# Optimization experiments

Hardware: AMD Instinct MI355X
Metric: run time of the kernel (lower is better)

The kernel has to match this reference:

```python
import jax, jax.numpy as jnp
import numpy as np

N = 100000   # nodes
E = 1000000  # edges
DIN = 128    # atom_in_features
DE = 16      # edge_attr_dim
H = 128      # hidden width (preprocess/cheb/postprocess)
K = 3        # Chebyshev order
EPS = 1e-5


def setup_inputs() -> dict:
    key = jax.random.key(0)
    ks = jax.random.split(key, 16)
    s = 0.02
    return {
        "x": jax.random.normal(ks[0], (N, DIN), jnp.float32),
        "edge_index": jax.random.randint(ks[1], (2, E), 0, N),
        "edge_attr": jax.random.normal(ks[2], (E, DE), jnp.float32),
        # AtomEdgeInteraction linear: (DIN+DE) -> H
        "w_int": jax.random.normal(ks[3], (DIN + DE, H), jnp.float32) * s,
        "b_int": jnp.zeros((H,), jnp.float32),
        # preprocess layer 1: Linear + BatchNorm + ReLU
        "w_pre": jax.random.normal(ks[4], (H, H), jnp.float32) * s,
        "b_pre": jnp.zeros((H,), jnp.float32),
        "g_pre": jnp.ones((H,), jnp.float32),
        "be_pre": jnp.zeros((H,), jnp.float32),
        # ChebConv layers: weight [K, in, out] + bias
        "cheb1_w": jax.random.normal(ks[5], (K, H, H), jnp.float32) * s,
        "cheb1_b": jnp.zeros((H,), jnp.float32),
        "cheb2_w": jax.random.normal(ks[6], (K, H, H), jnp.float32) * s,
        "cheb2_b": jnp.zeros((H,), jnp.float32),
        # postprocess: Linear + BatchNorm + ReLU
        "w_post": jax.random.normal(ks[7], (H, H), jnp.float32) * s,
        "b_post": jnp.zeros((H,), jnp.float32),
        "g_post": jnp.ones((H,), jnp.float32),
        "be_post": jnp.zeros((H,), jnp.float32),
        # output layer H -> 1
        "w_out": jax.random.normal(ks[8], (H, 1), jnp.float32) * s,
        "b_out": jnp.zeros((1,), jnp.float32),
    }


def _bn(z, g, b):
    # BatchNorm1d, training-mode batch statistics (biased variance, like torch)
    m = z.mean(0)
    v = ((z - m) ** 2).mean(0)
    return g * (z - m) * jax.lax.rsqrt(v + EPS) + b


def _cheb(h, W, b, row, col, norm):
    # ChebConv with sym normalization, lambda_max=2 => L_hat = -D^{-1/2} A D^{-1/2}
    def lhat(z):
        return jax.ops.segment_sum(norm[:, None] * z[row], col, num_segments=N)

    Tx0 = h
    out = Tx0 @ W[0]
    Tx1 = lhat(Tx0)
    out = out + Tx1 @ W[1]
    for k in range(2, W.shape[0]):
        Tx2 = 2.0 * lhat(Tx1) - Tx0
        out = out + Tx2 @ W[k]
        Tx0, Tx1 = Tx1, Tx2
    return out + b


def reference(x, edge_index, edge_attr,
              w_int, b_int,
              w_pre, b_pre, g_pre, be_pre,
              cheb1_w, cheb1_b, cheb2_w, cheb2_b,
              w_post, b_post, g_post, be_post,
              w_out, b_out):
    row, col = edge_index[0], edge_index[1]
    ones_e = jnp.ones((E,), x.dtype)

    # AtomEdgeInteraction: gather -> concat -> linear -> scatter_mean over col
    comb = jnp.concatenate([x[row], edge_attr], axis=-1)  # [E, DIN+DE]
    upd = comb @ w_int + b_int                             # [E, H]
    cnt = jax.ops.segment_sum(ones_e, col, num_segments=N)
    h = jax.ops.segment_sum(upd, col, num_segments=N) / jnp.clip(cnt, 1.0)[:, None]

    # preprocess layer 1 (Linear + BN + ReLU; dropout rate 0)
    h = jax.nn.relu(_bn(h @ w_pre + b_pre, g_pre, be_pre))

    # sym-normalized edge coefficients for scaled Laplacian
    deg = jax.ops.segment_sum(ones_e, row, num_segments=N)
    dis = jnp.where(deg > 0, jax.lax.rsqrt(jnp.maximum(deg, 1.0)), 0.0)
    norm = -dis[row] * dis[col]  # [E]

    h = jax.nn.relu(_cheb(h, cheb1_w, cheb1_b, row, col, norm))
    h = jax.nn.relu(_cheb(h, cheb2_w, cheb2_b, row, col, norm))

    # postprocess (Linear + BN + ReLU)
    h = jax.nn.relu(_bn(h @ w_post + b_post, g_post, be_post))

    # output layer, squeeze(-1) -> [N]
    return (h @ w_out + b_out).squeeze(-1)
```

## Files before the change

### kernel.cpp

```cpp
#include <hip/hip_runtime.h>
#include <hip/hip_bf16.h>

using u16 = unsigned short;
using u32 = unsigned int;

#define NN 100000
#define NE 1000000

typedef __attribute__((ext_vector_type(8))) short bfrag;
typedef __attribute__((ext_vector_type(4))) float ffrag;

#define BF16ONE2 0x3F803F80u

__device__ __forceinline__ float bf2f(u16 u) { return __uint_as_float(((u32)u) << 16); }
__device__ __forceinline__ u16 f2bf(float f) {
  u32 x = __float_as_uint(f);
  return (u16)((x + 0x7fffu + ((x >> 16) & 1u)) >> 16);
}
__device__ __forceinline__ float rdv(const void* p, long i, int f) {
  return f ? bf2f(((const u16*)p)[i]) : ((const float*)p)[i];
}
__device__ __forceinline__ void acc8(float* a, uint4 v, float w) {
  a[0] = fmaf(w, __uint_as_float(v.x << 16), a[0]);
  a[1] = fmaf(w, __uint_as_float(v.x & 0xffff0000u), a[1]);
  a[2] = fmaf(w, __uint_as_float(v.y << 16), a[2]);
  a[3] = fmaf(w, __uint_as_float(v.y & 0xffff0000u), a[3]);
  a[4] = fmaf(w, __uint_as_float(v.z << 16), a[4]);
  a[5] = fmaf(w, __uint_as_float(v.z & 0xffff0000u), a[5]);
  a[6] = fmaf(w, __uint_as_float(v.w << 16), a[6]);
  a[7] = fmaf(w, __uint_as_float(v.w & 0xffff0000u), a[7]);
}
__device__ __forceinline__ void acc8bn(float* a, uint4 v, float w, const float* A,
                                       const float* Bb) {
  float x;
  x = __uint_as_float(v.x << 16);
  a[0] = fmaf(w, fmaxf(fmaf(A[0], x, Bb[0]), 0.f), a[0]);
  x = __uint_as_float(v.x & 0xffff0000u);
  a[1] = fmaf(w, fmaxf(fmaf(A[1], x, Bb[1]), 0.f), a[1]);
  x = __uint_as_float(v.y << 16);
  a[2] = fmaf(w, fmaxf(fmaf(A[2], x, Bb[2]), 0.f), a[2]);
  x = __uint_as_float(v.y & 0xffff0000u);
  a[3] = fmaf(w, fmaxf(fmaf(A[3], x, Bb[3]), 0.f), a[3]);
  x = __uint_as_float(v.z << 16);
  a[4] = fmaf(w, fmaxf(fmaf(A[4], x, Bb[4]), 0.f), a[4]);
  x = __uint_as_float(v.z & 0xffff0000u);
  a[5] = fmaf(w, fmaxf(fmaf(A[5], x, Bb[5]), 0.f), a[5]);
  x = __uint_as_float(v.w << 16);
  a[6] = fmaf(w, fmaxf(fmaf(A[6], x, Bb[6]), 0.f), a[6]);
  x = __uint_as_float(v.w & 0xffff0000u);
  a[7] = fmaf(w, fmaxf(fmaf(A[7], x, Bb[7]), 0.f), a[7]);
}

#define OWXT 0
#define OWPRE 16384
#define OWD1 32768
#define OW11 49152
#define OV21 65536
#define OWD2 81920
#define OW12 98304
#define OV22 114688
#define OWPOST 131072
#define OWET 147456

#define ASTRIDE 136
#define ESTRIDE 132

struct PrepArgs { const void* in[16]; };

__global__ void k_prep(PrepArgs a, const u32* __restrict__ gp, u16* __restrict__ wq,
                       float* __restrict__ wf) {
  int t = blockIdx.x * 256 + threadIdx.x;
  int f = (gp[0] == BF16ONE2) ? 1 : 0;
  if (t < 16384) {
    int o = t >> 7, k = t & 127;
    int ko = k * 128 + o;
    int ok = o * 128 + k;
    wq[OWXT + ok] = f2bf(rdv(a.in[0], ko, f));
    wq[OWPRE + ok] = f2bf(rdv(a.in[2], ko, f));
    float c0 = rdv(a.in[6], ko, f);
    float c1 = rdv(a.in[6], 16384 + ko, f);
    float c2 = rdv(a.in[6], 32768 + ko, f);
    wq[OWD1 + ok] = f2bf(c0 - c2);
    wq[OW11 + ok] = f2bf(c1);
    wq[OV21 + ok] = f2bf(2.f * c2);
    float d0 = rdv(a.in[8], ko, f);
    float d1 = rdv(a.in[8], 16384 + ko, f);
    float d2 = rdv(a.in[8], 32768 + ko, f);
    wq[OWD2 + ok] = f2bf(d0 - d2);
    wq[OW12 + ok] = f2bf(d1);
    wq[OV22 + ok] = f2bf(2.f * d2);
    wq[OWPOST + ok] = f2bf(rdv(a.in[10], ko, f));
  }
  if (t < 4096) {
    int o = t >> 5, k = t & 31;
    wq[OWET + o * 32 + k] = (k < 16) ? f2bf(rdv(a.in[0], (long)(128 + k) * 128 + o, f)) : (u16)0;
  }
  if (t < 1281) {
    int s = t >> 7, j = t & 127;
    const int map[11] = {1, 3, 4, 5, 7, 9, 11, 12, 13, 14, 15};
    wf[t] = rdv(a.in[map[s]], j, f);
  }
}

__global__ void k_hist(const int* __restrict__ ei, int* cnt) {
  long t = (long)blockIdx.x * 256 + threadIdx.x;
  long e0 = t * 8;
  if (e0 + 8 <= NE) {
    int4 c0 = *(const int4*)(ei + NE + e0);
    int4 c1 = *(const int4*)(ei + NE + e0 + 4);
    atomicAdd(&cnt[c0.x], 1);
    atomicAdd(&cnt[c0.y], 1);
    atomicAdd(&cnt[c0.z], 1);
    atomicAdd(&cnt[c0.w], 1);
    atomicAdd(&cnt[c1.x], 1);
    atomicAdd(&cnt[c1.y], 1);
    atomicAdd(&cnt[c1.z], 1);
    atomicAdd(&cnt[c1.w], 1);
  } else {
    for (long e = e0; e < NE; e++) atomicAdd(&cnt[ei[NE + e]], 1);
  }
}

__global__ void k_scan1(const int* __restrict__ cnt, int* off, int* bsum) {
  __shared__ int s[1024];
  int t = threadIdx.x;
  int g = blockIdx.x * 1024 + t;
  int v = (g < NN) ? cnt[g] : 0;
  s[t] = v;
  __syncthreads();
  for (int st = 1; st < 1024; st <<= 1) {
    int x = (t >= st) ? s[t - st] : 0;
    __syncthreads();
    s[t] += x;
    __syncthreads();
  }
  if (g < NN) off[g] = s[t] - v;
  if (t == 1023) bsum[blockIdx.x] = s[t];
}

__global__ void k_scan23(int* off, const int* __restrict__ bsum, int* cur, int nb) {
  __shared__ int s[128];
  int t = threadIdx.x;
  int v = 0;
  if (t < 128) {
    v = (t < nb) ? bsum[t] : 0;
    s[t] = v;
  }
  __syncthreads();
  for (int st = 1; st < 128; st <<= 1) {
    int x = (t >= st && t < 128) ? s[t - st] : 0;
    __syncthreads();
    if (t < 128) s[t] += x;
    __syncthreads();
  }
  if (t < 128) s[t] -= v;
  __syncthreads();
  int pre = s[blockIdx.x];
  int g = blockIdx.x * 1024 + t;
  if (g < NN) {
    int o = off[g] + pre;
    off[g] = o;
    cur[g] = o;
  }
  if (g == 0) off[NN] = NE;
}

__global__ void k_place(const int* __restrict__ ei, int* cur, int* deg,
                        int2* __restrict__ cpk) {
  long t = (long)blockIdx.x * 256 + threadIdx.x;
  long e0 = t * 4;
  if (e0 + 4 <= NE) {
    int4 r4 = *(const int4*)(ei + e0);
    int4 c4 = *(const int4*)(ei + NE + e0);
    int p0 = atomicAdd(&cur[c4.x], 1);
    int p1 = atomicAdd(&cur[c4.y], 1);
    int p2 = atomicAdd(&cur[c4.z], 1);
    int p3 = atomicAdd(&cur[c4.w], 1);
    atomicAdd(&deg[r4.x], 1);
    atomicAdd(&deg[r4.y], 1);
    atomicAdd(&deg[r4.z], 1);
    atomicAdd(&deg[r4.w], 1);
    cpk[p0] = make_int2(r4.x, (int)e0);
    cpk[p1] = make_int2(r4.y, (int)e0 + 1);
    cpk[p2] = make_int2(r4.z, (int)e0 + 2);
    cpk[p3] = make_int2(r4.w, (int)e0 + 3);
  } else {
    for (long e = e0; e < NE; e++) {
      int rr = ei[e], cc = ei[NE + e];
      int p = atomicAdd(&cur[cc], 1);
      atomicAdd(&deg[rr], 1);
      cpk[p] = make_int2(rr, (int)e);
    }
  }
}

template <int BN>
__global__ __launch_bounds__(256) void k_spmm(const u16* __restrict__ src,
                                              u16* __restrict__ dst,
                                              const int* __restrict__ off,
                                              const int2* __restrict__ cpk,
                                              const float* __restrict__ cnorm,
                                              const float* __restrict__ ab) {
  int t = threadIdx.x;
  int node = blockIdx.x * 8 + (t >> 5);
  if (node >= NN) return;
  int l = t & 31;
  int half = l >> 4;
  int c = (l & 15) * 8;
  float A[8], Bb[8];
  if (BN) {
#pragma unroll
    for (int j = 0; j < 8; j++) {
      A[j] = ab[c + j];
      Bb[j] = ab[128 + c + j];
    }
  }
  int p0 = off[node], p1 = off[node + 1];
  float a[8];
#pragma unroll
  for (int j = 0; j < 8; j++) a[j] = 0.f;
  const u16* sp = src + c;
  for (int p = p0 + half; p < p1; p += 8) {
    int rr[4];
    float w[4];
#pragma unroll
    for (int u = 0; u < 4; u++) {
      int q = p + u * 2;
      int qc = q < p1 ? q : p1 - 1;
      rr[u] = cpk[qc].x;
      w[u] = (q < p1) ? cnorm[qc] : 0.f;
    }
#pragma unroll
    for (int u = 0; u < 4; u++) {
      uint4 v = *(const uint4*)(sp + (long)rr[u] * 128);
      if (BN) acc8bn(a, v, w[u], A, Bb);
      else acc8(a, v, w[u]);
    }
  }
#pragma unroll
  for (int j = 0; j < 8; j++) a[j] += __shfl_xor(a[j], 16);
  if (half) return;
  uint4 o;
  o.x = (u32)f2bf(a[0]) | ((u32)f2bf(a[1]) << 16);
  o.y = (u32)f2bf(a[2]) | ((u32)f2bf(a[3]) << 16);
  o.z = (u32)f2bf(a[4]) | ((u32)f2bf(a[5]) << 16);
  o.w = (u32)f2bf(a[6]) | ((u32)f2bf(a[7]) << 16);
  *(uint4*)(dst + (long)node * 128 + c) = o;
}

template <int WEIGHTED>
__device__ __forceinline__ void gather_lds(u16* sA, const u16* __restrict__ src,
                                           const int* __restrict__ off,
                                           const int2* __restrict__ cpk,
                                           const float* __restrict__ cnorm, int r0) {
  int tid = threadIdx.x;
  int grp = tid >> 4;
  int c = (tid & 15) * 8;
  const u16* sp = src + c;
#pragma unroll
  for (int i = 0; i < 4; i++) {
    int nl = grp * 4 + i;
    int node = r0 + nl;
    float a[8];
#pragma unroll
    for (int j = 0; j < 8; j++) a[j] = 0.f;
    if (node < NN) {
      int p0 = off[node], p1 = off[node + 1];
      for (int p = p0; p < p1; p += 8) {
        int rr[8];
        float w[8];
#pragma unroll
        for (int u = 0; u < 8; u++) {
          int q = p + u;
          int qc = q < p1 ? q : p1 - 1;
          rr[u] = cpk[qc].x;
          w[u] = (q < p1) ? (WEIGHTED ? cnorm[qc] : 1.f) : 0.f;
        }
#pragma unroll
        for (int u = 0; u < 8; u++)
          acc8(a, *(const uint4*)(sp + (long)rr[u] * 128), w[u]);
      }
    }
    uint4 o;
    o.x = (u32)f2bf(a[0]) | ((u32)f2bf(a[1]) << 16);
    o.y = (u32)f2bf(a[2]) | ((u32)f2bf(a[3]) << 16);
    o.z = (u32)f2bf(a[4]) | ((u32)f2bf(a[5]) << 16);
    o.w = (u32)f2bf(a[6]) | ((u32)f2bf(a[7]) << 16);
    *(uint4*)(sA + nl * ASTRIDE + c) = o;
  }
}

__global__ __launch_bounds__(256) void k_asum(const void* __restrict__ eattr,
                                              const u32* __restrict__ gp,
                                              u16* __restrict__ asum,
                                              const int* __restrict__ off,
                                              const int2* __restrict__ cpk,
                                              const int* __restrict__ deg,
                                              float* __restrict__ cnorm) {
  int t = blockIdx.x * 256 + threadIdx.x;
  int node = t >> 4;
  if (node >= NN) return;
  int j = t & 15;
  int p0 = off[node], p1 = off[node + 1];
  int dn = deg[node];
  float ndis = dn > 0 ? -rsqrtf((float)dn) : 0.f;
  for (int p = p0 + j; p < p1; p += 16)
    cnorm[p] = ndis * rsqrtf((float)deg[cpk[p].x]);
  float a = 0.f;
  if (gp[0] == BF16ONE2) {
    const u16* e16 = (const u16*)eattr;
    for (int p = p0; p < p1; p += 8) {
      float s[8];
#pragma unroll
      for (int u = 0; u < 8; u++) {
        int q = p + u;
        int qc = q < p1 ? q : p1 - 1;
        float v = bf2f(e16[(long)cpk[qc].y * 16 + j]);
        s[u] = (q < p1) ? v : 0.f;
      }
      a += ((s[0] + s[1]) + (s[2] + s[3])) + ((s[4] + s[5]) + (s[6] + s[7]));
    }
  } else {
    const float* e32 = (const float*)eattr;
    for (int p = p0; p < p1; p += 8) {
      float s[8];
#pragma unroll
      for (int u = 0; u < 8; u++) {
        int q = p + u;
        int qc = q < p1 ? q : p1 - 1;
        float v = e32[(long)cpk[qc].y * 16 + j];
        s[u] = (q < p1) ? v : 0.f;
      }
      a += ((s[0] + s[1]) + (s[2] + s[3])) + ((s[4] + s[5]) + (s[6] + s[7]));
    }
  }
  asum[(long)node * 16 + j] = f2bf(a);
}

struct MArgs {
  const void* A0; const u16* W0T; int a0raw;
  const float* bias;
  u16* out;
  const u32* gp;
  float* part;
};

__global__ __launch_bounds__(256) void k_mgemm(MArgs m) {
  constexpr int ROWS = 128, RT = 8, TPR = 2, SEGW = 64;
  __shared__ __align__(16) u16 sA[ROWS * ASTRIDE];
  int tid = threadIdx.x;
  int wv = tid >> 6, lane = tid & 63;
  int col16 = lane & 15, quad = lane >> 4;
  int r0 = blockIdx.x * ROWS;

  ffrag acc[RT * 2];
#pragma unroll
  for (int i = 0; i < RT * 2; i++)
#pragma unroll
    for (int g = 0; g < 4; g++) acc[i][g] = 0.f;

  {
    int row = tid / TPR, seg = tid % TPR;
    int ra = r0 + row;
    if (ra >= NN) ra = NN - 1;
    bool f32a = m.a0raw && (m.gp[0] != BF16ONE2);
    if (f32a) {
      const float* gs = (const float*)m.A0 + (long)ra * 128 + seg * SEGW;
      u32* lp = (u32*)(sA + row * ASTRIDE + seg * SEGW);
#pragma unroll
      for (int e = 0; e < SEGW / 8; e++) {
        float4 v0 = *(const float4*)(gs + e * 8);
        float4 v1 = *(const float4*)(gs + e * 8 + 4);
        lp[e * 4 + 0] = (u32)f2bf(v0.x) | ((u32)f2bf(v0.y) << 16);
        lp[e * 4 + 1] = (u32)f2bf(v0.z) | ((u32)f2bf(v0.w) << 16);
        lp[e * 4 + 2] = (u32)f2bf(v1.x) | ((u32)f2bf(v1.y) << 16);
        lp[e * 4 + 3] = (u32)f2bf(v1.z) | ((u32)f2bf(v1.w) << 16);
      }
    } else {
      const u16* gs = (const u16*)m.A0 + (long)ra * 128 + seg * SEGW;
      uint4* lp = (uint4*)(sA + row * ASTRIDE + seg * SEGW);
#pragma unroll
      for (int e = 0; e < SEGW / 8; e++) lp[e] = *(const uint4*)(gs + e * 8);
    }
  }
  bfrag b0[2][4];
#pragma unroll
  for (int c = 0; c < 2; c++)
#pragma unroll
    for (int kb = 0; kb < 4; kb++)
      b0[c][kb] = *(const bfrag*)(m.W0T + (long)(wv * 32 + c * 16 + col16) * 128 + kb * 32 + quad * 8);
  __syncthreads();
#pragma unroll
  for (int kb = 0; kb < 4; kb++)
#pragma unroll
    for (int rt = 0; rt < RT; rt++) {
      bfrag af = *(const bfrag*)(sA + (rt * 16 + col16) * ASTRIDE + kb * 32 + quad * 8);
      acc[rt * 2 + 0] = __builtin_amdgcn_mfma_f32_16x16x32_bf16(af, b0[0][kb], acc[rt * 2 + 0], 0, 0, 0);
      acc[rt * 2 + 1] = __builtin_amdgcn_mfma_f32_16x16x32_bf16(af, b0[1][kb], acc[rt * 2 + 1], 0, 0, 0);
    }
  __syncthreads();
#pragma unroll
  for (int rt = 0; rt < RT; rt++)
#pragma unroll
    for (int c = 0; c < 2; c++) {
      int col = wv * 32 + c * 16 + col16;
      float bj = m.bias ? m.bias[col] : 0.f;
#pragma unroll
      for (int g = 0; g < 4; g++)
        sA[(rt * 16 + quad * 4 + g) * ESTRIDE + col] = f2bf(acc[rt * 2 + c][g] + bj);
    }
  __syncthreads();
  {
    int rr = tid / TPR, d = tid % TPR;
    int rowg = r0 + rr;
    if (rowg < NN) {
      const u16* sp2 = sA + rr * ESTRIDE + d * 64;
      uint4* o = (uint4*)(m.out + (long)rowg * 128 + d * 64);
#pragma unroll
      for (int e = 0; e < 8; e++) {
        const uint2* s2 = (const uint2*)(sp2 + e * 8);
        uint2 lo = s2[0], hi = s2[1];
        o[e] = make_uint4(lo.x, lo.y, hi.x, hi.y);
      }
    }
  }
  if (m.part) {
    __shared__ float ps[256], pq[256];
    int col = tid & 127, hf = tid >> 7;
    float s = 0.f, q = 0.f;
#pragma unroll
    for (int r = 0; r < 64; r++) {
      int rr = hf * 64 + r;
      if (r0 + rr < NN) {
        float v = bf2f(sA[rr * ESTRIDE + col]);
        s += v;
        q += v * v;
      }
    }
    ps[tid] = s;
    pq[tid] = q;
    __syncthreads();
    if (tid < 128) {
      m.part[(long)blockIdx.x * 256 + tid] = ps[tid] + ps[tid + 128];
      m.part[(long)blockIdx.x * 256 + 128 + tid] = pq[tid] + pq[tid + 128];
    }
  }
}

__global__ __launch_bounds__(256) void k_etpre(const u16* __restrict__ Xg,
                                               const u16* __restrict__ asum,
                                               const u16* __restrict__ Wet,
                                               const u16* __restrict__ Wpre,
                                               const float* __restrict__ b_int,
                                               const float* __restrict__ b_pre,
                                               const int* __restrict__ off,
                                               const int2* __restrict__ cpk,
                                               u16* __restrict__ out, float* part) {
  __shared__ __align__(16) u16 sA[64 * ASTRIDE];
  __shared__ __align__(16) u16 sE[64 * 32];
  int tid = threadIdx.x;
  int wv = tid >> 6, lane = tid & 63;
  int col16 = lane & 15, quad = lane >> 4;
  int r0 = blockIdx.x * 64;

  gather_lds<0>(sA, Xg, off, cpk, nullptr, r0);
  {
    int row = tid >> 2, seg = tid & 3;
    int ra = r0 + row;
    if (ra >= NN) ra = NN - 1;
    if (seg < 2)
      *(uint4*)(sE + row * 32 + seg * 8) = *(const uint4*)(asum + (long)ra * 16 + seg * 8);
    else
      *(uint4*)(sE + row * 32 + seg * 8) = make_uint4(0, 0, 0, 0);
  }
  bfrag be[2];
#pragma unroll
  for (int c = 0; c < 2; c++)
    be[c] = *(const bfrag*)(Wet + (long)(wv * 32 + c * 16 + col16) * 32 + quad * 8);
  __syncthreads();
  ffrag accE[8];
#pragma unroll
  for (int i = 0; i < 8; i++)
#pragma unroll
    for (int g = 0; g < 4; g++) accE[i][g] = 0.f;
#pragma unroll
  for (int rt = 0; rt < 4; rt++) {
    bfrag af = *(const bfrag*)(sE + (rt * 16 + col16) * 32 + quad * 8);
    accE[rt * 2 + 0] = __builtin_amdgcn_mfma_f32_16x16x32_bf16(af, be[0], accE[rt * 2 + 0], 0, 0, 0);
    accE[rt * 2 + 1] = __builtin_amdgcn_mfma_f32_16x16x32_bf16(af, be[1], accE[rt * 2 + 1], 0, 0, 0);
  }
#pragma unroll
  for (int rt = 0; rt < 4; rt++)
#pragma unroll
    for (int g = 0; g < 4; g++) {
      int rr = rt * 16 + quad * 4 + g;
      int r = r0 + rr;
      int cc = (r < NN) ? off[r + 1] - off[r] : 0;
      float inv = 1.f / (float)(cc > 1 ? cc : 1);
#pragma unroll
      for (int c = 0; c < 2; c++) {
        int col = wv * 32 + c * 16 + col16;
        float bj = b_int[col];
        float v = accE[rt * 2 + c][g] + bf2f(sA[rr * ASTRIDE + col]);
        v = (v + (float)cc * bj) * inv;
        sA[rr * ASTRIDE + col] = f2bf(v);
      }
    }
  bfrag b1[2][4];
#pragma unroll
  for (int c = 0; c < 2; c++)
#pragma unroll
    for (int kb = 0; kb < 4; kb++)
      b1[c][kb] = *(const bfrag*)(Wpre + (long)(wv * 32 + c * 16 + col16) * 128 + kb * 32 + quad * 8);
  __syncthreads();
  ffrag a2[8];
#pragma unroll
  for (int i = 0; i < 8; i++)
#pragma unroll
    for (int g = 0; g < 4; g++) a2[i][g] = 0.f;
#pragma unroll
  for (int kb = 0; kb < 4; kb++)
#pragma unroll
    for (int rt = 0; rt < 4; rt++) {
      bfrag af = *(const bfrag*)(sA + (rt * 16 + col16) * ASTRIDE + kb * 32 + quad * 8);
      a2[rt * 2 + 0] = __builtin_amdgcn_mfma_f32_16x16x32_bf16(af, b1[0][kb], a2[rt * 2 + 0], 0, 0, 0);
      a2[rt * 2 + 1] = __builtin_amdgcn_mfma_f32_16x16x32_bf16(af, b1[1][kb], a2[rt * 2 + 1], 0, 0, 0);
    }
  __syncthreads();
#pragma unroll
  for (int rt = 0; rt < 4; rt++)
#pragma unroll
    for (int c = 0; c < 2; c++) {
      int col = wv * 32 + c * 16 + col16;
      float bj = b_pre[col];
#pragma unroll
      for (int g = 0; g < 4; g++)
        sA[(rt * 16 + quad * 4 + g) * ESTRIDE + col] = f2bf(a2[rt * 2 + c][g] + bj);
    }
  __syncthreads();
  {
    int rr = tid >> 2, d = tid & 3;
    int rowg = r0 + rr;
    if (rowg < NN) {
      const u16* sp2 = sA + rr * ESTRIDE + d * 32;
      uint4* o = (uint4*)(out + (long)rowg * 128 + d * 32);
#pragma unroll
      for (int e = 0; e < 4; e++) {
        const uint2* s2 = (const uint2*)(sp2 + e * 8);
        uint2 lo = s2[0], hi = s2[1];
        o[e] = make_uint4(lo.x, lo.y, hi.x, hi.y);
      }
    }
  }
  {
    __shared__ float ps[256], pq[256];
    int col = tid & 127, hf = tid >> 7;
    float s = 0.f, q = 0.f;
#pragma unroll
    for (int r = 0; r < 32; r++) {
      int rr = hf * 32 + r;
      if (r0 + rr < NN) {
        float v = bf2f(sA[rr * ESTRIDE + col]);
        s += v;
        q += v * v;
      }
    }
    ps[tid] = s;
    pq[tid] = q;
    __syncthreads();
    if (tid < 128) {
      part[(long)blockIdx.x * 256 + tid] = ps[tid] + ps[tid + 128];
      part[(long)blockIdx.x * 256 + 128 + tid] = pq[tid] + pq[tid + 128];
    }
  }
}

template <int BN>
__global__ __launch_bounds__(256) void k_cheb(const u16* __restrict__ hb,
                                              const u16* __restrict__ T1,
                                              const int* __restrict__ off,
                                              const int2* __restrict__ cpk,
                                              const float* __restrict__ cnorm,
                                              const u16* __restrict__ WD,
                                              const u16* __restrict__ W1,
                                              const u16* __restrict__ V2,
                                              const float* __restrict__ bias,
                                              const float* __restrict__ ab,
                                              u16* __restrict__ out) {
  __shared__ __align__(16) u16 sA[64 * ASTRIDE];
  int tid = threadIdx.x;
  int wv = tid >> 6, lane = tid & 63;
  int col16 = lane & 15, quad = lane >> 4;
  int r0 = blockIdx.x * 64;

  gather_lds<1>(sA, T1, off, cpk, cnorm, r0);
  bfrag bv[2][4];
#pragma unroll
  for (int c = 0; c < 2; c++)
#pragma unroll
    for (int kb = 0; kb < 4; kb++)
      bv[c][kb] = *(const bfrag*)(V2 + (long)(wv * 32 + c * 16 + col16) * 128 + kb * 32 + quad * 8);
  __syncthreads();
  ffrag acc[8];
#pragma unroll
  for (int i = 0; i < 8; i++)
#pragma unroll
    for (int g = 0; g < 4; g++) acc[i][g] = 0.f;
#pragma unroll
  for (int kb = 0; kb < 4; kb++)
#pragma unroll
    for (int rt = 0; rt < 4; rt++) {
      bfrag af = *(const bfrag*)(sA + (rt * 16 + col16) * ASTRIDE + kb * 32 + quad * 8);
      acc[rt * 2 + 0] = __builtin_amdgcn_mfma_f32_16x16x32_bf16(af, bv[0][kb], acc[rt * 2 + 0], 0, 0, 0);
      acc[rt * 2 + 1] = __builtin_amdgcn_mfma_f32_16x16x32_bf16(af, bv[1][kb], acc[rt * 2 + 1], 0, 0, 0);
    }
  __syncthreads();

  {
    int row = tid >> 2, seg = tid & 3;
    int ra = r0 + row;
    if (ra >= NN) ra = NN - 1;
    const u16* gs = hb + (long)ra * 128 + seg * 32;
    uint4* lp = (uint4*)(sA + row * ASTRIDE + seg * 32);
    if (BN) {
#pragma unroll
      for (int e = 0; e < 4; e++) {
        uint4 v = *(const uint4*)(gs + e * 8);
        int cb = seg * 32 + e * 8;
        float f0 = fmaxf(fmaf(ab[cb + 0], __uint_as_float(v.x << 16), ab[128 + cb + 0]), 0.f);
        float f1 = fmaxf(fmaf(ab[cb + 1], __uint_as_float(v.x & 0xffff0000u), ab[128 + cb + 1]), 0.f);
        float f2 = fmaxf(fmaf(ab[cb + 2], __uint_as_float(v.y << 16), ab[128 + cb + 2]), 0.f);
        float f3 = fmaxf(fmaf(ab[cb + 3], __uint_as_float(v.y & 0xffff0000u), ab[128 + cb + 3]), 0.f);
        float f4 = fmaxf(fmaf(ab[cb + 4], __uint_as_float(v.z << 16), ab[128 + cb + 4]), 0.f);
        float f5 = fmaxf(fmaf(ab[cb + 5], __uint_as_float(v.z & 0xffff0000u), ab[128 + cb + 5]), 0.f);
        float f6 = fmaxf(fmaf(ab[cb + 6], __uint_as_float(v.w << 16), ab[128 + cb + 6]), 0.f);
        float f7 = fmaxf(fmaf(ab[cb + 7], __uint_as_float(v.w & 0xffff0000u), ab[128 + cb + 7]), 0.f);
        uint4 o;
        o.x = (u32)f2bf(f0) | ((u32)f2bf(f1) << 16);
        o.y = (u32)f2bf(f2) | ((u32)f2bf(f3) << 16);
        o.z = (u32)f2bf(f4) | ((u32)f2bf(f5) << 16);
        o.w = (u32)f2bf(f6) | ((u32)f2bf(f7) << 16);
        lp[e] = o;
      }
    } else {
#pragma unroll
      for (int e = 0; e < 4; e++) lp[e] = *(const uint4*)(gs + e * 8);
    }
  }
#pragma unroll
  for (int c = 0; c < 2; c++)
#pragma unroll
    for (int kb = 0; kb < 4; kb++)
      bv[c][kb] = *(const bfrag*)(WD + (long)(wv * 32 + c * 16 + col16) * 128 + kb * 32 + quad * 8);
  __syncthreads();
#pragma unroll
  for (int kb = 0; kb < 4; kb++)
#pragma unroll
    for (int rt = 0; rt < 4; rt++) {
      bfrag af = *(const bfrag*)(sA + (rt * 16 + col16) * ASTRIDE + kb * 32 + quad * 8);
      acc[rt * 2 + 0] = __builtin_amdgcn_mfma_f32_16x16x32_bf16(af, bv[0][kb], acc[rt * 2 + 0], 0, 0, 0);
      acc[rt * 2 + 1] = __builtin_amdgcn_mfma_f32_16x16x32_bf16(af, bv[1][kb], acc[rt * 2 + 1], 0, 0, 0);
    }
  __syncthreads();

  {
    int row = tid >> 2, seg = tid & 3;
    int ra = r0 + row;
    if (ra >= NN) ra = NN - 1;
    const u16* gs = T1 + (long)ra * 128 + seg * 32;
    uint4* lp = (uint4*)(sA + row * ASTRIDE + seg * 32);
#pragma unroll
    for (int e = 0; e < 4; e++) lp[e] = *(const uint4*)(gs + e * 8);
  }
#pragma unroll
  for (int c = 0; c < 2; c++)
#pragma unroll
    for (int kb = 0; kb < 4; kb++)
      bv[c][kb] = *(const bfrag*)(W1 + (long)(wv * 32 + c * 16 + col16) * 128 + kb * 32 + quad * 8);
  __syncthreads();
#pragma unroll
  for (int kb = 0; kb < 4; kb++)
#pragma unroll
    for (int rt = 0; rt < 4; rt++) {
      bfrag af = *(const bfrag*)(sA + (rt * 16 + col16) * ASTRIDE + kb * 32 + quad * 8);
      acc[rt * 2 + 0] = __builtin_amdgcn_mfma_f32_16x16x32_bf16(af, bv[0][kb], acc[rt * 2 + 0], 0, 0, 0);
      acc[rt * 2 + 1] = __builtin_amdgcn_mfma_f32_16x16x32_bf16(af, bv[1][kb], acc[rt * 2 + 1], 0, 0, 0);
    }
  __syncthreads();

#pragma unroll
  for (int rt = 0; rt < 4; rt++)
#pragma unroll
    for (int c = 0; c < 2; c++) {
      int col = wv * 32 + c * 16 + col16;
      float bj = bias[col];
#pragma unroll
      for (int g = 0; g < 4; g++)
        sA[(rt * 16 + quad * 4 + g) * ESTRIDE + col] = f2bf(fmaxf(acc[rt * 2 + c][g] + bj, 0.f));
    }
  __syncthreads();
  {
    int rr = tid >> 2, d = tid & 3;
    int rowg = r0 + rr;
    if (rowg < NN) {
      const u16* sp2 = sA + rr * ESTRIDE + d * 32;
      uint4* o = (uint4*)(out + (long)rowg * 128 + d * 32);
#pragma unroll
      for (int e = 0; e < 4; e++) {
        const uint2* s2 = (const uint2*)(sp2 + e * 8);
        uint2 lo = s2[0], hi = s2[1];
        o[e] = make_uint4(lo.x, lo.y, hi.x, hi.y);
      }
    }
  }
}

__global__ void k_redfin(const float* __restrict__ part, const float* __restrict__ gamma,
                         const float* __restrict__ beta, float* ab, int nblk) {
  int tid = threadIdx.x;
  int col = blockIdx.x * 16 + (tid & 15);
  int ch = tid >> 4;
  float s = 0.f, q = 0.f;
  for (int b = ch; b < nblk; b += 16) {
    s += part[(long)b * 256 + col];
    q += part[(long)b * 256 + 128 + col];
  }
  __shared__ float sh[256], qh[256];
  sh[tid] = s;
  qh[tid] = q;
  __syncthreads();
  if (tid < 16) {
    float ts = 0.f, tq = 0.f;
#pragma unroll
    for (int i = 0; i < 16; i++) {
      ts += sh[i * 16 + tid];
      tq += qh[i * 16 + tid];
    }
    int j = blockIdx.x * 16 + tid;
    float m = ts * (1.f / (float)NN);
    float v = fmaxf(tq * (1.f / (float)NN) - m * m, 0.f);
    float a = gamma[j] * rsqrtf(v + 1e-5f);
    ab[j] = a;
    ab[128 + j] = beta[j] - m * a;
  }
}

__global__ void k_out(const u16* __restrict__ z, const float* __restrict__ ab,
                      const float* __restrict__ wout, const float* __restrict__ bout,
                      const u32* __restrict__ gp, void* __restrict__ y) {
  int node = blockIdx.x * 4 + (threadIdx.x >> 6);
  if (node >= NN) return;
  int lane = threadIdx.x & 63;
  float s = 0.f;
#pragma unroll
  for (int c = lane; c < 128; c += 64) {
    float zz = bf2f(z[(long)node * 128 + c]);
    float h = fmaxf(ab[c] * zz + ab[128 + c], 0.f);
    s += h * wout[c];
  }
#pragma unroll
  for (int o = 32; o > 0; o >>= 1) s += __shfl_down(s, o);
  if (lane == 0) {
    float r = s + bout[0];
    if (gp[0] == BF16ONE2) ((u16*)y)[node] = f2bf(r);
    else ((float*)y)[node] = r;
  }
}

extern "C" void kernel_launch(void* const* d_in, const int* in_sizes, int n_in,
                              void* d_out, int out_size, void* d_ws, size_t ws_size,
                              hipStream_t stream) {
  const void* x = d_in[0];
  const int* ei = (const int*)d_in[1];
  const void* eattr = d_in[2];
  const u32* gp = (const u32*)d_in[7];
  (void)in_sizes; (void)n_in; (void)out_size; (void)ws_size;

  char* w = (char*)d_ws;
  size_t p = 0;
  auto alloc = [&](size_t b) { size_t r = p; p += (b + 255) & ~(size_t)255; return r; };
  size_t o_cnt = alloc((size_t)NN * 4);
  size_t o_deg = alloc((size_t)NN * 4);
  size_t o_zero_end = p;
  size_t o_cur = alloc((size_t)NN * 4);
  size_t o_off = alloc((size_t)(NN + 1) * 4);
  size_t o_bsum = alloc(1024 * 4);
  size_t o_ab = alloc(512 * 4);
  size_t o_wq = alloc((size_t)151552 * 2);
  size_t o_wf = alloc((size_t)1281 * 4);
  size_t o_cpk = alloc((size_t)NE * 8);
  size_t o_cnrm = alloc((size_t)NE * 4);
  size_t o_asum = alloc((size_t)NN * 16 * 2);
  size_t o_part = alloc((size_t)1563 * 256 * 4);
  size_t o_Bx = alloc((size_t)NN * 128 * 2);
  size_t o_Bt = alloc((size_t)NN * 128 * 2);

  int* cnt = (int*)(w + o_cnt);
  int* deg = (int*)(w + o_deg);
  int* cur = (int*)(w + o_cur);
  int* off = (int*)(w + o_off);
  int* bsum = (int*)(w + o_bsum);
  float* abA = (float*)(w + o_ab);
  float* abB = abA + 256;
  u16* wq = (u16*)(w + o_wq);
  float* wf = (float*)(w + o_wf);
  int2* cpk = (int2*)(w + o_cpk);
  float* cnrm = (float*)(w + o_cnrm);
  u16* asum = (u16*)(w + o_asum);
  float* part = (float*)(w + o_part);
  u16* Bx = (u16*)(w + o_Bx);
  u16* Bt = (u16*)(w + o_Bt);

  hipMemsetAsync(w + o_cnt, 0, o_zero_end - o_cnt, stream);

  int gH = (NE / 8 + 255) / 256;
  int gP = (NE / 4 + 255) / 256;
  int nb = (NN + 1023) / 1024;
  int gS = (NN + 7) / 8;
  int gG1 = (NN + 127) / 128;
  int gG2 = (NN + 63) / 64;

  {
    PrepArgs a;
    for (int i = 0; i < 16; i++) a.in[i] = d_in[3 + i];
    k_prep<<<64, 256, 0, stream>>>(a, gp, wq, wf);
  }

  k_hist<<<gH, 256, 0, stream>>>(ei, cnt);
  k_scan1<<<nb, 1024, 0, stream>>>(cnt, off, bsum);
  k_scan23<<<nb, 1024, 0, stream>>>(off, bsum, cur, nb);
  k_place<<<gP, 256, 0, stream>>>(ei, cur, deg, cpk);
  k_asum<<<(NN * 16 + 255) / 256, 256, 0, stream>>>(eattr, gp, asum, off, cpk, deg, cnrm);

  {
    MArgs a = {};
    a.A0 = x; a.W0T = wq + OWXT; a.a0raw = 1;
    a.out = Bx; a.gp = gp;
    k_mgemm<<<gG1, 256, 0, stream>>>(a);
  }
  k_etpre<<<gG2, 256, 0, stream>>>(Bx, asum, wq + OWET, wq + OWPRE, wf + 0, wf + 128,
                                   off, cpk, Bt, part);
  k_redfin<<<8, 256, 0, stream>>>(part, wf + 256, wf + 384, abA, gG2);

  k_spmm<1><<<gS, 256, 0, stream>>>(Bt, Bx, off, cpk, cnrm, abA);
  k_cheb<1><<<gG2, 256, 0, stream>>>(Bt, Bx, off, cpk, cnrm,
                                     wq + OWD1, wq + OW11, wq + OV21, wf + 512, abA, Bt);

  k_spmm<0><<<gS, 256, 0, stream>>>(Bt, Bx, off, cpk, cnrm, nullptr);
  k_cheb<0><<<gG2, 256, 0, stream>>>(Bt, Bx, off, cpk, cnrm,
                                     wq + OWD2, wq + OW12, wq + OV22, wf + 640, nullptr, Bt);

  {
    MArgs a = {};
    a.A0 = Bt; a.W0T = wq + OWPOST;
    a.bias = wf + 768; a.out = Bx; a.gp = gp; a.part = part;
    k_mgemm<<<gG1, 256, 0, stream>>>(a);
  }
  k_redfin<<<8, 256, 0, stream>>>(part, wf + 896, wf + 1024, abB, gG1);
  k_out<<<(NN + 3) / 4, 256, 0, stream>>>(Bx, abB, wf + 1152, wf + 1280, gp, d_out);
}
```

Measured before the change: 739.4 us.

## Replace global-atomic CSR build with two-level bucketed counting sort

Swaps the global-atomic histogram, scan and placement used to build the column-sorted edge list (and the row degree count) for a two-pass radix-style counting sort. Edges are first bucketed by the high bits of the node id using shared-memory histograms per block, then each bucket is finely sorted in shared memory to produce offsets and packed (row, edge) pairs. This removes heavy contended global atomics and the memset, at the cost of more kernel launches and extra scratch traffic, with scratch reusing the Bx buffer. Within-node edge order may now differ from before.

```diff
diff --git a/kernel.cpp b/kernel.cpp
--- a/kernel.cpp
+++ b/kernel.cpp
@@ -6,6 +6,8 @@
 
 #define NN 100000
 #define NE 1000000
+#define NBKT 196
+#define NBLK 489
 
 typedef __attribute__((ext_vector_type(8))) short bfrag;
 typedef __attribute__((ext_vector_type(4))) float ffrag;
@@ -102,96 +104,159 @@
   }
 }
 
-__global__ void k_hist(const int* __restrict__ ei, int* cnt) {
-  long t = (long)blockIdx.x * 256 + threadIdx.x;
-  long e0 = t * 8;
-  if (e0 + 8 <= NE) {
-    int4 c0 = *(const int4*)(ei + NE + e0);
-    int4 c1 = *(const int4*)(ei + NE + e0 + 4);
-    atomicAdd(&cnt[c0.x], 1);
-    atomicAdd(&cnt[c0.y], 1);
-    atomicAdd(&cnt[c0.z], 1);
-    atomicAdd(&cnt[c0.w], 1);
-    atomicAdd(&cnt[c1.x], 1);
-    atomicAdd(&cnt[c1.y], 1);
-    atomicAdd(&cnt[c1.z], 1);
-    atomicAdd(&cnt[c1.w], 1);
-  } else {
-    for (long e = e0; e < NE; e++) atomicAdd(&cnt[ei[NE + e]], 1);
-  }
-}
-
-__global__ void k_scan1(const int* __restrict__ cnt, int* off, int* bsum) {
-  __shared__ int s[1024];
+
+__global__ void k_cnt(const int* __restrict__ ei, int* __restrict__ bcnt,
+                      int* __restrict__ rbcnt) {
+  __shared__ int hc[NBKT], hr[NBKT];
+  int t = threadIdx.x, blk = blockIdx.x;
+  for (int i = t; i < NBKT; i += 256) { hc[i] = 0; hr[i] = 0; }
+  __syncthreads();
+  long base = (long)blk * 2048;
+#pragma unroll
+  for (int i = 0; i < 8; i++) {
+    long e = base + i * 256 + t;
+    if (e < NE) {
+      atomicAdd(&hc[ei[NE + e] >> 9], 1);
+      atomicAdd(&hr[ei[e] >> 9], 1);
+    }
+  }
+  __syncthreads();
+  for (int i = t; i < NBKT; i += 256) {
+    bcnt[i * NBLK + blk] = hc[i];
+    rbcnt[i * NBLK + blk] = hr[i];
+  }
+}
+
+__global__ void k_bscan(int* __restrict__ bcnt, int* __restrict__ rbcnt,
+                        int* __restrict__ btot) {
+  __shared__ int ss[256];
+  int j = blockIdx.x, t = threadIdx.x;
+  int* arr = ((j < NBKT) ? bcnt : rbcnt) + (j % NBKT) * NBLK;
+  int a = (2 * t < NBLK) ? arr[2 * t] : 0;
+  int b = (2 * t + 1 < NBLK) ? arr[2 * t + 1] : 0;
+  ss[t] = a + b;
+  __syncthreads();
+  for (int st = 1; st < 256; st <<= 1) {
+    int x = (t >= st) ? ss[t - st] : 0;
+    __syncthreads();
+    ss[t] += x;
+    __syncthreads();
+  }
+  int base = ss[t] - a - b;
+  if (2 * t < NBLK) arr[2 * t] = base;
+  if (2 * t + 1 < NBLK) arr[2 * t + 1] = base + a;
+  if (t == 255) btot[j] = ss[255];
+}
+
+__global__ void k_bbase(const int* __restrict__ btot, int* __restrict__ bbase,
+                        int* __restrict__ rbbase, int* __restrict__ off) {
+  __shared__ int ss[256];
   int t = threadIdx.x;
-  int g = blockIdx.x * 1024 + t;
-  int v = (g < NN) ? cnt[g] : 0;
-  s[t] = v;
-  __syncthreads();
-  for (int st = 1; st < 1024; st <<= 1) {
-    int x = (t >= st) ? s[t - st] : 0;
+  int v = (t < NBKT) ? btot[t] : 0;
+  ss[t] = v;
+  __syncthreads();
+  for (int st = 1; st < 256; st <<= 1) {
+    int x = (t >= st) ? ss[t - st] : 0;
     __syncthreads();
-    s[t] += x;
+    ss[t] += x;
     __syncthreads();
   }
-  if (g < NN) off[g] = s[t] - v;
-  if (t == 1023) bsum[blockIdx.x] = s[t];
-}
-
-__global__ void k_scan23(int* off, const int* __restrict__ bsum, int* cur, int nb) {
-  __shared__ int s[128];
-  int t = threadIdx.x;
-  int v = 0;
-  if (t < 128) {
-    v = (t < nb) ? bsum[t] : 0;
-    s[t] = v;
-  }
-  __syncthreads();
-  for (int st = 1; st < 128; st <<= 1) {
-    int x = (t >= st && t < 128) ? s[t - st] : 0;
+  if (t < NBKT) bbase[t] = ss[t] - v;
+  if (t == NBKT - 1) bbase[NBKT] = ss[t];
+  __syncthreads();
+  int v2 = (t < NBKT) ? btot[NBKT + t] : 0;
+  ss[t] = v2;
+  __syncthreads();
+  for (int st = 1; st < 256; st <<= 1) {
+    int x = (t >= st) ? ss[t - st] : 0;
     __syncthreads();
-    if (t < 128) s[t] += x;
+    ss[t] += x;
     __syncthreads();
   }
-  if (t < 128) s[t] -= v;
-  __syncthreads();
-  int pre = s[blockIdx.x];
-  int g = blockIdx.x * 1024 + t;
-  if (g < NN) {
-    int o = off[g] + pre;
-    off[g] = o;
-    cur[g] = o;
-  }
-  if (g == 0) off[NN] = NE;
-}
-
-__global__ void k_place(const int* __restrict__ ei, int* cur, int* deg,
-                        int2* __restrict__ cpk) {
-  long t = (long)blockIdx.x * 256 + threadIdx.x;
-  long e0 = t * 4;
-  if (e0 + 4 <= NE) {
-    int4 r4 = *(const int4*)(ei + e0);
-    int4 c4 = *(const int4*)(ei + NE + e0);
-    int p0 = atomicAdd(&cur[c4.x], 1);
-    int p1 = atomicAdd(&cur[c4.y], 1);
-    int p2 = atomicAdd(&cur[c4.z], 1);
-    int p3 = atomicAdd(&cur[c4.w], 1);
-    atomicAdd(&deg[r4.x], 1);
-    atomicAdd(&deg[r4.y], 1);
-    atomicAdd(&deg[r4.z], 1);
-    atomicAdd(&deg[r4.w], 1);
-    cpk[p0] = make_int2(r4.x, (int)e0);
-    cpk[p1] = make_int2(r4.y, (int)e0 + 1);
-    cpk[p2] = make_int2(r4.z, (int)e0 + 2);
-    cpk[p3] = make_int2(r4.w, (int)e0 + 3);
-  } else {
-    for (long e = e0; e < NE; e++) {
-      int rr = ei[e], cc = ei[NE + e];
-      int p = atomicAdd(&cur[cc], 1);
-      atomicAdd(&deg[rr], 1);
-      cpk[p] = make_int2(rr, (int)e);
-    }
-  }
+  if (t < NBKT) rbbase[t] = ss[t] - v2;
+  if (t == NBKT - 1) rbbase[NBKT] = ss[t];
+  if (t == 0) off[NN] = NE;
+}
+
+__global__ void k_scat(const int* __restrict__ ei, const int* __restrict__ bofs,
+                       const int* __restrict__ rbofs, const int* __restrict__ bbase,
+                       const int* __restrict__ rbbase, u32* __restrict__ sle,
+                       u32* __restrict__ srow, u16* __restrict__ srl) {
+  __shared__ int cc[NBKT], cr[NBKT], cbase[NBKT], rbase[NBKT];
+  int t = threadIdx.x, blk = blockIdx.x;
+  for (int i = t; i < NBKT; i += 256) {
+    cc[i] = 0;
+    cr[i] = 0;
+    cbase[i] = bbase[i] + bofs[i * NBLK + blk];
+    rbase[i] = rbbase[i] + rbofs[i * NBLK + blk];
+  }
+  __syncthreads();
+  long base = (long)blk * 2048;
+#pragma unroll
+  for (int i = 0; i < 8; i++) {
+    long e = base + i * 256 + t;
+    if (e < NE) {
+      int c = ei[NE + e], r = ei[e];
+      int k1 = atomicAdd(&cc[c >> 9], 1);
+      int d1 = cbase[c >> 9] + k1;
+      sle[d1] = ((u32)(c & 511) << 20) | (u32)e;
+      srow[d1] = (u32)r;
+      int k2 = atomicAdd(&cr[r >> 9], 1);
+      int d2 = rbase[r >> 9] + k2;
+      srl[d2] = (u16)(r & 511);
+    }
+  }
+}
+
+__global__ void k_fine(const u32* __restrict__ sle, const u32* __restrict__ srow,
+                       const int* __restrict__ bbase, int* __restrict__ off,
+                       int2* __restrict__ cpk) {
+  __shared__ u32 hist[512];
+  __shared__ u32 ss[256];
+  int t = threadIdx.x, b = blockIdx.x;
+  hist[t] = 0;
+  hist[t + 256] = 0;
+  __syncthreads();
+  int lo = bbase[b], hi = bbase[b + 1];
+  for (int p = lo + t; p < hi; p += 256) atomicAdd(&hist[sle[p] >> 20], 1);
+  __syncthreads();
+  u32 a = hist[2 * t], bb = hist[2 * t + 1];
+  ss[t] = a + bb;
+  __syncthreads();
+  for (int st = 1; st < 256; st <<= 1) {
+    u32 x = (t >= st) ? ss[t - st] : 0;
+    __syncthreads();
+    ss[t] += x;
+    __syncthreads();
+  }
+  u32 base = ss[t] - a - bb;
+  u32 c0 = (u32)lo + base, c1 = (u32)lo + base + a;
+  hist[2 * t] = c0;
+  hist[2 * t + 1] = c1;
+  int col0 = b * 512 + 2 * t, col1 = col0 + 1;
+  if (col0 < NN) off[col0] = (int)c0;
+  if (col1 < NN) off[col1] = (int)c1;
+  __syncthreads();
+  for (int p = lo + t; p < hi; p += 256) {
+    u32 v = sle[p];
+    u32 pos = atomicAdd(&hist[v >> 20], 1);
+    cpk[pos] = make_int2((int)srow[p], (int)(v & 0xFFFFFu));
+  }
+}
+
+__global__ void k_deg(const u16* __restrict__ srl, const int* __restrict__ rbbase,
+                      int* __restrict__ deg) {
+  __shared__ int hist[512];
+  int t = threadIdx.x, b = blockIdx.x;
+  hist[t] = 0;
+  hist[t + 256] = 0;
+  __syncthreads();
+  int lo = rbbase[b], hi = rbbase[b + 1];
+  for (int p = lo + t; p < hi; p += 256) atomicAdd(&hist[srl[p]], 1);
+  __syncthreads();
+  int n0 = b * 512 + t, n1 = n0 + 256;
+  if (n0 < NN) deg[n0] = hist[t];
+  if (n1 < NN) deg[n1] = hist[t + 256];
 }
 
 template <int BN>
@@ -779,12 +844,13 @@
   char* w = (char*)d_ws;
   size_t p = 0;
   auto alloc = [&](size_t b) { size_t r = p; p += (b + 255) & ~(size_t)255; return r; };
-  size_t o_cnt = alloc((size_t)NN * 4);
   size_t o_deg = alloc((size_t)NN * 4);
-  size_t o_zero_end = p;
-  size_t o_cur = alloc((size_t)NN * 4);
   size_t o_off = alloc((size_t)(NN + 1) * 4);
-  size_t o_bsum = alloc(1024 * 4);
+  size_t o_bcnt = alloc((size_t)NBKT * NBLK * 4);
+  size_t o_rbcnt = alloc((size_t)NBKT * NBLK * 4);
+  size_t o_btot = alloc((size_t)2 * NBKT * 4);
+  size_t o_bbase = alloc((size_t)(NBKT + 1) * 4);
+  size_t o_rbbase = alloc((size_t)(NBKT + 1) * 4);
   size_t o_ab = alloc(512 * 4);
   size_t o_wq = alloc((size_t)151552 * 2);
   size_t o_wf = alloc((size_t)1281 * 4);
@@ -795,11 +861,13 @@
   size_t o_Bx = alloc((size_t)NN * 128 * 2);
   size_t o_Bt = alloc((size_t)NN * 128 * 2);
 
-  int* cnt = (int*)(w + o_cnt);
   int* deg = (int*)(w + o_deg);
-  int* cur = (int*)(w + o_cur);
   int* off = (int*)(w + o_off);
-  int* bsum = (int*)(w + o_bsum);
+  int* bcnt = (int*)(w + o_bcnt);
+  int* rbcnt = (int*)(w + o_rbcnt);
+  int* btot = (int*)(w + o_btot);
+  int* bbase = (int*)(w + o_bbase);
+  int* rbbase = (int*)(w + o_rbbase);
   float* abA = (float*)(w + o_ab);
   float* abB = abA + 256;
   u16* wq = (u16*)(w + o_wq);
@@ -810,12 +878,10 @@
   float* part = (float*)(w + o_part);
   u16* Bx = (u16*)(w + o_Bx);
   u16* Bt = (u16*)(w + o_Bt);
-
-  hipMemsetAsync(w + o_cnt, 0, o_zero_end - o_cnt, stream);
-
-  int gH = (NE / 8 + 255) / 256;
-  int gP = (NE / 4 + 255) / 256;
-  int nb = (NN + 1023) / 1024;
+  u32* sle = (u32*)Bx;
+  u32* srow = sle + NE;
+  u16* srl = (u16*)(srow + NE);
+
   int gS = (NN + 7) / 8;
   int gG1 = (NN + 127) / 128;
   int gG2 = (NN + 63) / 64;
@@ -826,10 +892,13 @@
     k_prep<<<64, 256, 0, stream>>>(a, gp, wq, wf);
   }
 
-  k_hist<<<gH, 256, 0, stream>>>(ei, cnt);
-  k_scan1<<<nb, 1024, 0, stream>>>(cnt, off, bsum);
-  k_scan23<<<nb, 1024, 0, stream>>>(off, bsum, cur, nb);
-  k_place<<<gP, 256, 0, stream>>>(ei, cur, deg, cpk);
+  k_cnt<<<NBLK, 256, 0, stream>>>(ei, bcnt, rbcnt);
+  k_bscan<<<2 * NBKT, 256, 0, stream>>>(bcnt, rbcnt, btot);
+  k_bbase<<<1, 256, 0, stream>>>(btot, bbase, rbbase, off);
+  k_scat<<<NBLK, 256, 0, stream>>>(ei, bcnt, rbcnt, bbase, rbbase, sle, srow, srl);
+  k_fine<<<NBKT, 256, 0, stream>>>(sle, srow, bbase, off, cpk);
+  k_deg<<<NBKT, 256, 0, stream>>>(srl, rbbase, deg);
+
   k_asum<<<(NN * 16 + 255) / 256, 256, 0, stream>>>(eattr, gp, asum, off, cpk, deg, cnrm);
 
   {
```

After: 671.1 us. 9.2% less time.
